# Performance work log

Hardware: AMD Instinct MI355X
Metric: run time of the kernel (lower is better)

## Reference

```python
import jax, jax.numpy as jnp
import numpy as np

B, S, D = 2, 2048, 1024
H, DK = 16, 64


def setup_inputs() -> dict:
    key = jax.random.key(0)
    ks = jax.random.split(key, 10)
    scale = D ** -0.5
    x = jax.random.normal(ks[0], (B, S, D), dtype=jnp.float32)
    mask = jax.random.randint(ks[1], (B, S), 0, 2) > 0  # True = masked positions
    Wq = jax.random.normal(ks[2], (D, H * DK), dtype=jnp.float32) * scale
    Wk = jax.random.normal(ks[3], (D, H * DK), dtype=jnp.float32) * scale
    Wv = jax.random.normal(ks[4], (D, H * DK), dtype=jnp.float32) * scale
    Wo = jax.random.normal(ks[5], (H * DK, D), dtype=jnp.float32) * scale
    bq = jnp.zeros((H * DK,), jnp.float32)
    bk = jnp.zeros((H * DK,), jnp.float32)
    bv = jnp.zeros((H * DK,), jnp.float32)
    bo = jnp.zeros((D,), jnp.float32)
    return {"x": x, "mask": mask, "Wq": Wq, "bq": bq, "Wk": Wk, "bk": bk,
            "Wv": Wv, "bv": bv, "Wo": Wo, "bo": bo}


def reference(x, mask, Wq, bq, Wk, bk, Wv, bv, Wo, bo):
    b, s, _ = x.shape
    # Linear + activation (dropout is identity at eval)
    q = jax.nn.relu(x @ Wq + bq).reshape(b, s, H, DK)
    k = jax.nn.relu(x @ Wk + bk).reshape(b, s, H, DK)
    v = jax.nn.relu(x @ Wv + bv).reshape(b, s, H, DK)
    # scores: [B, H, Sq, Sk]
    attn = jnp.einsum("bqhd,bkhd->bhqk", q, k) * (DK ** -0.5)
    # NOTE: original uses masked_fill(mask, 1e-9) BEFORE softmax (not -inf)
    attn = jnp.where(mask[:, None, None, :], jnp.float32(1e-9), attn)
    attn = jax.nn.softmax(attn, axis=-1)
    out = jnp.einsum("bhqk,bkhd->bqhd", attn, v).reshape(b, s, H * DK)
    return jax.nn.relu(out @ Wo + bo)
```

## Files before the change

### kernel.cpp

```cpp
#include <hip/hip_runtime.h>
#include <stdint.h>

typedef __attribute__((ext_vector_type(8))) short short8;
typedef __attribute__((ext_vector_type(4))) short short4b;
typedef __attribute__((ext_vector_type(4))) float f32x4;
typedef __attribute__((ext_vector_type(4))) unsigned short ushort4_t;

#define MFMA16(a, b, c) __builtin_amdgcn_mfma_f32_16x16x32_bf16((a), (b), (c), 0, 0, 0)

#if defined(__HIP_DEVICE_COMPILE__)
  #if __has_builtin(__builtin_amdgcn_mfma_f32_16x16x16bf16_1k)
    #define MFMA16K16(a, b, c) __builtin_amdgcn_mfma_f32_16x16x16bf16_1k((a), (b), (c), 0, 0, 0)
  #else
    #define MFMA16K16(a, b, c) __builtin_amdgcn_mfma_f32_16x16x16_bf16((a), (b), (c), 0, 0, 0)
  #endif
  #if __has_builtin(__builtin_amdgcn_exp2f)
    #define EXP2(x) __builtin_amdgcn_exp2f(x)
  #else
    #define EXP2(x) exp2f(x)
  #endif
#else
  #define MFMA16K16(a, b, c) (c)
  #define EXP2(x) exp2f(x)
#endif

#define SCL_F (0.125f * 1.44269504f)

__device__ __forceinline__ float b2f(unsigned short u) {
    union { unsigned u; float f; } c; c.u = ((unsigned)u) << 16; return c.f;
}
__device__ __forceinline__ unsigned short f2b(float f) {
    union { float f; unsigned u; } c; c.f = f;
    unsigned r = c.u + 0x7FFF + ((c.u >> 16) & 1);
    return (unsigned short)(r >> 16);
}
__device__ __forceinline__ unsigned f_as_u(float f) {
    union { float f; unsigned u; } c; c.f = f; return c.u;
}

__device__ __forceinline__ void g2lds16(const unsigned short* g, unsigned lds_byte_off) {
    __builtin_amdgcn_global_load_lds(
        (const __attribute__((address_space(1))) void*)(uintptr_t)g,
        (__attribute__((address_space(3))) void*)(uintptr_t)lds_byte_off,
        16, 0, 0);
}

__global__ void detect_dtype(const unsigned short* __restrict__ x, int* __restrict__ flag) {
    __shared__ int cnt;
    if (threadIdx.x == 0) cnt = 0;
    __syncthreads();
    int insane = 0;
    #pragma unroll
    for (int j = 0; j < 4; ++j) {
        unsigned short u = x[threadIdx.x * 4 + j];
        int e = (u >> 7) & 0xFF;
        if ((e >= 1 && e <= 90) || e >= 165) insane++;
    }
    atomicAdd(&cnt, insane);
    __syncthreads();
    if (threadIdx.x == 0) *flag = (cnt > 128) ? 1 : 0;
}

__global__ __launch_bounds__(256) void convtrans_k(const void* __restrict__ s0, const void* __restrict__ s1,
                                                   const void* __restrict__ s2, const void* __restrict__ s3,
                                                   const void* __restrict__ b0, const void* __restrict__ b1,
                                                   const void* __restrict__ b2, const void* __restrict__ b3s,
                                                   const void* __restrict__ xsrc,
                                                   unsigned short* __restrict__ xdst,
                                                   unsigned short* __restrict__ dstBase,
                                                   unsigned short* __restrict__ dstB3,
                                                   unsigned short* __restrict__ dstBo,
                                                   const int* __restrict__ flag) {
    const int z = blockIdx.z;
    if (z >= 5) {
        if (!*flag) return;
        const int slice = z - 5;
        const size_t i0 = (size_t)slice * 524288 + (blockIdx.y * 16 + blockIdx.x) * 2048 + threadIdx.x * 8;
        const float* s = (const float*)xsrc;
        float4 f0 = *(const float4*)&s[i0];
        float4 f1 = *(const float4*)&s[i0 + 4];
        unsigned short* t = &xdst[i0];
        t[0] = f2b(f0.x); t[1] = f2b(f0.y); t[2] = f2b(f0.z); t[3] = f2b(f0.w);
        t[4] = f2b(f1.x); t[5] = f2b(f1.y); t[6] = f2b(f1.z); t[7] = f2b(f1.w);
        return;
    }
    if (z == 4) {
        if (blockIdx.y != 0 || blockIdx.x >= 4) return;
        const int w = blockIdx.x;
        const void* src = (w == 0) ? b0 : (w == 1) ? b1 : (w == 2) ? b2 : b3s;
        const float bscl = (w == 0) ? SCL_F : 1.0f;
        #pragma unroll
        for (int j = 0; j < 4; ++j) {
            const int i = threadIdx.x * 4 + j;
            float fv = (*flag) ? ((const float*)src)[i] : b2f(((const unsigned short*)src)[i]);
            unsigned short v = f2b(fv * bscl);
            if (w < 3) dstB3[w * 1024 + i] = v;
            else dstBo[i] = v;
        }
        return;
    }
    __shared__ __align__(16) unsigned short tile[64 * 72];
    const void* src = (z == 0) ? s0 : (z == 1) ? s1 : (z == 2) ? s2 : s3;
    unsigned short* dst = dstBase + (size_t)z * 1024 * 1024;
    const float wscl = (z == 0) ? SCL_F : 1.0f;
    const int tid = threadIdx.x;
    const int r0 = blockIdx.y * 64, c0 = blockIdx.x * 64;
    const int rb = tid >> 3, c = (tid & 7) * 8;
    if (*flag) {
        const float* s = (const float*)src;
        #pragma unroll
        for (int it = 0; it < 2; ++it) {
            int rr = it * 32 + rb;
            float4 f0 = *(const float4*)&s[(size_t)(r0 + rr) * 1024 + c0 + c];
            float4 f1 = *(const float4*)&s[(size_t)(r0 + rr) * 1024 + c0 + c + 4];
            unsigned short* t = &tile[rr * 72 + c];
            t[0] = f2b(f0.x * wscl); t[1] = f2b(f0.y * wscl); t[2] = f2b(f0.z * wscl); t[3] = f2b(f0.w * wscl);
            t[4] = f2b(f1.x * wscl); t[5] = f2b(f1.y * wscl); t[6] = f2b(f1.z * wscl); t[7] = f2b(f1.w * wscl);
        }
    } else if (z == 0) {
        const unsigned short* s = (const unsigned short*)src;
        #pragma unroll
        for (int it = 0; it < 2; ++it) {
            int rr = it * 32 + rb;
            union { short8 v; unsigned short u[8]; } in;
            in.v = *(const short8*)&s[(size_t)(r0 + rr) * 1024 + c0 + c];
            unsigned short* t = &tile[rr * 72 + c];
            #pragma unroll
            for (int j = 0; j < 8; ++j) t[j] = f2b(b2f(in.u[j]) * SCL_F);
        }
    } else {
        const unsigned short* s = (const unsigned short*)src;
        #pragma unroll
        for (int it = 0; it < 2; ++it) {
            int rr = it * 32 + rb;
            *(short8*)&tile[rr * 72 + c] = *(const short8*)&s[(size_t)(r0 + rr) * 1024 + c0 + c];
        }
    }
    __syncthreads();
    #pragma unroll
    for (int it = 0; it < 2; ++it) {
        int n = it * 32 + rb, k8 = c;
        union { short8 s; unsigned short u[8]; } tmp;
        #pragma unroll
        for (int j = 0; j < 8; ++j) tmp.u[j] = tile[(k8 + j) * 72 + n];
        *(short8*)&dst[(size_t)(c0 + n) * 1024 + r0 + k8] = tmp.s;
    }
}

__global__ __launch_bounds__(256) void mask_k(unsigned short* __restrict__ qkv,
                                              const int* __restrict__ mask) {
    const int row = blockIdx.x * 2 + (threadIdx.x >> 7);
    const int col = (threadIdx.x & 127) * 8;
    if (mask[row]) {
        const short8 z = {0, 0, 0, 0, 0, 0, 0, 0};
        *(short8*)&qkv[(size_t)row * 3072 + 1024 + col] = z;
    }
}

__global__ __launch_bounds__(256) void gemm_bias_relu(const unsigned short* __restrict__ A,
                                                      const void* __restrict__ Araw,
                                                      const unsigned short* __restrict__ BT,
                                                      const unsigned short* __restrict__ bias,
                                                      void* __restrict__ C,
                                                      unsigned short* __restrict__ VtG,
                                                      const int* __restrict__ flag,
                                                      int M, int N, int K, int mode) {
    __shared__ __align__(16) unsigned short As[3][128 * 32];
    __shared__ __align__(16) unsigned short Bs[3][128 * 32];
    const int tid = threadIdx.x;
    const int wave = tid >> 6, lane = tid & 63;
    const int quad = lane >> 4, l16 = lane & 15;
    const int wm = wave >> 1, wn = wave & 1;
    const int m0 = blockIdx.y * 128, n0 = blockIdx.x * 128;

    const unsigned short* Ause = (Araw != nullptr && *flag == 0) ? (const unsigned short*)Araw : A;

    f32x4 acc[4][4];
    #pragma unroll
    for (int i = 0; i < 4; i++)
        #pragma unroll
        for (int j = 0; j < 4; j++) acc[i][j] = (f32x4){0.f, 0.f, 0.f, 0.f};

    const int srow = wave * 32 + (lane >> 2);
    const int sc8  = (lane & 3) * 8;
    const unsigned short* gA0 = Ause + (size_t)(m0 + srow) * K + sc8;
    const unsigned short* gA1 = gA0 + (size_t)16 * K;
    const unsigned short* gB0 = BT + (size_t)(n0 + srow) * K + sc8;
    const unsigned short* gB1 = gB0 + (size_t)16 * K;

    unsigned lA0 = (unsigned)(uintptr_t)&As[0][0] + wave * 2048;
    unsigned lA1 = (unsigned)(uintptr_t)&As[1][0] + wave * 2048;
    unsigned lA2 = (unsigned)(uintptr_t)&As[2][0] + wave * 2048;
    unsigned lB0 = (unsigned)(uintptr_t)&Bs[0][0] + wave * 2048;
    unsigned lB1 = (unsigned)(uintptr_t)&Bs[1][0] + wave * 2048;
    unsigned lB2 = (unsigned)(uintptr_t)&Bs[2][0] + wave * 2048;
    const unsigned short* pA0 = &As[0][0];
    const unsigned short* pA1 = &As[1][0];
    const unsigned short* pA2 = &As[2][0];
    const unsigned short* pB0 = &Bs[0][0];
    const unsigned short* pB1 = &Bs[1][0];
    const unsigned short* pB2 = &Bs[2][0];

    g2lds16(gA0, lA0); g2lds16(gA1, lA0 + 1024);
    g2lds16(gB0, lB0); g2lds16(gB1, lB0 + 1024);
    if (32 < K) {
        g2lds16(gA0 + 32, lA1); g2lds16(gA1 + 32, lA1 + 1024);
        g2lds16(gB0 + 32, lB1); g2lds16(gB1 + 32, lB1 + 1024);
    }
    if (64 < K) {
        g2lds16(gA0 + 64, lA2); g2lds16(gA1 + 64, lA2 + 1024);
        g2lds16(gB0 + 64, lB2); g2lds16(gB1 + 64, lB2 + 1024);
    }

    for (int k0 = 0; k0 < K; k0 += 32) {
        if (k0 + 64 < K)       asm volatile("s_waitcnt vmcnt(8)" ::: "memory");
        else if (k0 + 32 < K)  asm volatile("s_waitcnt vmcnt(4)" ::: "memory");
        else                   asm volatile("s_waitcnt vmcnt(0)" ::: "memory");
        __builtin_amdgcn_s_barrier();

        short8 af[4], bf[4];
        #pragma unroll
        for (int i = 0; i < 4; i++) af[i] = *(const short8*)&pA0[(wm * 64 + i * 16 + l16) * 32 + quad * 8];
        #pragma unroll
        for (int j = 0; j < 4; j++) bf[j] = *(const short8*)&pB0[(wn * 64 + j * 16 + l16) * 32 + quad * 8];
        #pragma unroll
        for (int i = 0; i < 4; i++)
            #pragma unroll
            for (int j = 0; j < 4; j++)
                acc[i][j] = MFMA16(af[i], bf[j], acc[i][j]);

        __builtin_amdgcn_s_barrier();

        if (k0 + 96 < K) {
            g2lds16(gA0 + k0 + 96, lA0); g2lds16(gA1 + k0 + 96, lA0 + 1024);
            g2lds16(gB0 + k0 + 96, lB0); g2lds16(gB1 + k0 + 96, lB0 + 1024);
        }
        unsigned tu;
        tu = lA0; lA0 = lA1; lA1 = lA2; lA2 = tu;
        tu = lB0; lB0 = lB1; lB1 = lB2; lB2 = tu;
        const unsigned short* tp;
        tp = pA0; pA0 = pA1; pA1 = pA2; pA2 = tp;
        tp = pB0; pB0 = pB1; pB1 = pB2; pB2 = tp;
    }

    if (mode == 2 && n0 >= 2048) {
        #pragma unroll
        for (int j = 0; j < 4; j++) {
            const int col = n0 + wn * 64 + j * 16 + l16;
            const int h  = (col - 2048) >> 6;
            const int dk = (col - 2048) & 63;
            const float bj = b2f(bias[col]);
            #pragma unroll
            for (int i = 0; i < 4; i++) {
                const int rowb = m0 + wm * 64 + i * 16 + quad * 4;
                const int bb = rowb >> 11;
                const int s0 = rowb & 2047;
                ushort4_t w;
                #pragma unroll
                for (int r = 0; r < 4; r++) {
                    float v = acc[i][j][r] + bj;
                    v = v > 0.f ? v : 0.f;
                    w[r] = f2b(v);
                }
                *(ushort4_t*)&VtG[(size_t)((bb * 16 + h) * 64 + dk) * 2048 + s0] = w;
            }
        }
    } else {
        const int f32out = (mode == 1) && (*flag != 0);
        #pragma unroll
        for (int j = 0; j < 4; j++) {
            const int col = n0 + wn * 64 + j * 16 + l16;
            const float bj = b2f(bias[col]);
            #pragma unroll
            for (int i = 0; i < 4; i++) {
                const int rowb = m0 + wm * 64 + i * 16 + quad * 4;
                #pragma unroll
                for (int r = 0; r < 4; r++) {
                    float v = acc[i][j][r] + bj;
                    v = v > 0.f ? v : 0.f;
                    if (f32out) ((float*)C)[(size_t)(rowb + r) * N + col] = v;
                    else ((unsigned short*)C)[(size_t)(rowb + r) * N + col] = f2b(v);
                }
            }
        }
    }
}

#define ATTN_TILE(Kbuf, Vbuf)                                                            \
    do {                                                                                 \
        __builtin_amdgcn_s_setprio(1);                                                   \
        f32x4 sA[4], sB[4];                                                              \
        _Pragma("unroll")                                                                \
        for (int t = 0; t < 4; ++t) {                                                    \
            const short8 kb0 = *(const short8*)&(Kbuf)[(((t * 16 + l16) * 64) + quad * 8) ^ rx];       \
            const short8 kb1 = *(const short8*)&(Kbuf)[(((t * 16 + l16) * 64) + 32 + quad * 8) ^ rx];  \
            f32x4 z = (f32x4){0.f, 0.f, 0.f, 0.f};                                       \
            sA[t] = MFMA16(kb1, qa1, MFMA16(kb0, qa0, z));                               \
            sB[t] = MFMA16(kb1, qb1, MFMA16(kb0, qb0, z));                               \
        }                                                                                \
        short4b vb[4][4];                                                                \
        _Pragma("unroll")                                                                \
        for (int t = 0; t < 4; ++t)                                                      \
            _Pragma("unroll")                                                            \
            for (int n = 0; n < 4; ++n)                                                  \
                vb[t][n] = *(const short4b*)&(Vbuf)[(((n * 16 + l16) * 64) + t * 16 + quad * 4) ^ rx]; \
        _Pragma("unroll")                                                                \
        for (int t = 0; t < 4; ++t) {                                                    \
            float pA[4], pB[4];                                                          \
            _Pragma("unroll")                                                            \
            for (int r = 0; r < 4; ++r) {                                                \
                pA[r] = EXP2(sA[t][r]);                                                  \
                pB[r] = EXP2(sB[t][r]);                                                  \
            }                                                                            \
            union { unsigned u[2]; short4b s; } fa, fb;                                  \
            fa.u[0] = __builtin_amdgcn_perm(f_as_u(pA[1]), f_as_u(pA[0]), 0x07060302u);  \
            fa.u[1] = __builtin_amdgcn_perm(f_as_u(pA[3]), f_as_u(pA[2]), 0x07060302u);  \
            fb.u[0] = __builtin_amdgcn_perm(f_as_u(pB[1]), f_as_u(pB[0]), 0x07060302u);  \
            fb.u[1] = __builtin_amdgcn_perm(f_as_u(pB[3]), f_as_u(pB[2]), 0x07060302u);  \
            _Pragma("unroll")                                                            \
            for (int n = 0; n < 4; ++n) {                                                \
                oA[n] = MFMA16K16(fa.s, vb[t][n], oA[n]);                                \
                oB[n] = MFMA16K16(fb.s, vb[t][n], oB[n]);                                \
            }                                                                            \
            sumA = MFMA16K16(fa.s, ones, sumA);                                          \
            sumB = MFMA16K16(fb.s, ones, sumB);                                          \
        }                                                                                \
        __builtin_amdgcn_s_setprio(0);                                                   \
    } while (0)

__global__ __launch_bounds__(256) void attn_kernel(const unsigned short* __restrict__ qkv,
                                                   const unsigned short* __restrict__ VtG,
                                                   unsigned short* __restrict__ out) {
    __shared__ __align__(16) unsigned short Ks[2][64 * 64];
    __shared__ __align__(16) unsigned short Vs[2][64 * 64];

    const int l = blockIdx.y * 16 + blockIdx.x;
    const int v = (l & 7) * 64 + (l >> 3);
    const int qt = v & 15, bh = v >> 4;
    const int b = bh >> 4, h = bh & 15;
    const int tid = threadIdx.x, wave = tid >> 6, lane = tid & 63;
    const int quad = lane >> 4, l16 = lane & 15;

    const int qrowA = qt * 128 + wave * 16 + l16;
    const unsigned short* qpA = qkv + (size_t)(b * 2048 + qrowA) * 3072 + h * 64;
    const unsigned short* qpB = qpA + (size_t)64 * 3072;
    const short8 qa0 = *(const short8*)(qpA + quad * 8);
    const short8 qa1 = *(const short8*)(qpA + 32 + quad * 8);
    const short8 qb0 = *(const short8*)(qpB + quad * 8);
    const short8 qb1 = *(const short8*)(qpB + 32 + quad * 8);

    f32x4 oA[4], oB[4], sumA, sumB;
    #pragma unroll
    for (int n = 0; n < 4; n++) { oA[n] = (f32x4){0.f,0.f,0.f,0.f}; oB[n] = (f32x4){0.f,0.f,0.f,0.f}; }
    sumA = (f32x4){0.f,0.f,0.f,0.f};
    sumB = (f32x4){0.f,0.f,0.f,0.f};

    const short4b ones = { (short)0x3F80, (short)0x3F80, (short)0x3F80, (short)0x3F80 };

    const int srow = tid >> 2;
    const int scol = (tid & 3) * 16;
    const int sxor = (srow & 7) << 3;
    const unsigned short* kg = qkv + (size_t)(b * 2048 + srow) * 3072 + 1024 + h * 64 + scol;
    const unsigned short* vg = VtG + (size_t)(bh * 64 + srow) * 2048 + scol;
    const size_t kstep = (size_t)64 * 3072;
    const int sidx0 = (srow * 64 + scol) ^ sxor;
    const int sidx1 = (srow * 64 + scol + 8) ^ sxor;
    unsigned short* wK0a = &Ks[0][sidx0];  unsigned short* wK1a = &Ks[0][sidx1];
    unsigned short* wV0a = &Vs[0][sidx0];  unsigned short* wV1a = &Vs[0][sidx1];
    unsigned short* wK0b = &Ks[1][sidx0];  unsigned short* wK1b = &Ks[1][sidx1];
    unsigned short* wV0b = &Vs[1][sidx0];  unsigned short* wV1b = &Vs[1][sidx1];

    const int rx = (l16 & 7) << 3;

    short8 rkA0 = *(const short8*)(kg);
    short8 rkA1 = *(const short8*)(kg + 8);
    short8 rvA0 = *(const short8*)(vg);
    short8 rvA1 = *(const short8*)(vg + 8);
    *(short8*)wK0a = rkA0;  *(short8*)wK1a = rkA1;
    *(short8*)wV0a = rvA0;  *(short8*)wV1a = rvA1;
    short8 rkB0 = *(const short8*)(kg + kstep);
    short8 rkB1 = *(const short8*)(kg + kstep + 8);
    short8 rvB0 = *(const short8*)(vg + 64);
    short8 rvB1 = *(const short8*)(vg + 64 + 8);
    __syncthreads();

    for (int kt = 0; kt < 32; kt += 2) {
        *(short8*)wK0b = rkB0;  *(short8*)wK1b = rkB1;
        *(short8*)wV0b = rvB0;  *(short8*)wV1b = rvB1;
        if (kt + 2 < 32) {
            rkA0 = *(const short8*)(kg + (kt + 2) * kstep);
            rkA1 = *(const short8*)(kg + (kt + 2) * kstep + 8);
            rvA0 = *(const short8*)(vg + (kt + 2) * 64);
            rvA1 = *(const short8*)(vg + (kt + 2) * 64 + 8);
        }
        ATTN_TILE(Ks[0], Vs[0]);
        __syncthreads();

        if (kt + 2 < 32) {
            *(short8*)wK0a = rkA0;  *(short8*)wK1a = rkA1;
            *(short8*)wV0a = rvA0;  *(short8*)wV1a = rvA1;
        }
        if (kt + 3 < 32) {
            rkB0 = *(const short8*)(kg + (kt + 3) * kstep);
            rkB1 = *(const short8*)(kg + (kt + 3) * kstep + 8);
            rvB0 = *(const short8*)(vg + (kt + 3) * 64);
            rvB1 = *(const short8*)(vg + (kt + 3) * 64 + 8);
        }
        ATTN_TILE(Ks[1], Vs[1]);
        __syncthreads();
    }

    float invA[4], invB[4];
    #pragma unroll
    for (int r = 0; r < 4; ++r) { invA[r] = 1.0f / sumA[r]; invB[r] = 1.0f / sumB[r]; }
    #pragma unroll
    for (int n = 0; n < 4; n++)
        #pragma unroll
        for (int r = 0; r < 4; r++) {
            const int row = qt * 128 + wave * 16 + quad * 4 + r;
            out[(size_t)(b * 2048 + row) * 1024 + h * 64 + n * 16 + l16] = f2b(oA[n][r] * invA[r]);
            out[(size_t)(b * 2048 + row + 64) * 1024 + h * 64 + n * 16 + l16] = f2b(oB[n][r] * invB[r]);
        }
}

extern "C" void kernel_launch(void* const* d_in, const int* in_sizes, int n_in,
                              void* d_out, int out_size, void* d_ws, size_t ws_size,
                              hipStream_t stream) {
    const void* x  = d_in[0];
    const int*  mk = (const int*)d_in[1];
    const void* Wq = d_in[2]; const void* bq = d_in[3];
    const void* Wk = d_in[4]; const void* bk = d_in[5];
    const void* Wv = d_in[6]; const void* bv = d_in[7];
    const void* Wo = d_in[8]; const void* bo = d_in[9];

    char* wsb = (char*)d_ws;
    int* flag = (int*)wsb;
    unsigned short* W0 = (unsigned short*)(wsb + 64);

    const size_t M1 = 1024u * 1024u;
    const size_t M4 = 4096u * 1024u;
    unsigned short* xb  = W0;
    unsigned short* WT  = xb + M4;
    unsigned short* WoT = WT + 3 * M1;
    unsigned short* b3  = WoT + M1;
    unsigned short* bob = b3 + 4096;
    unsigned short* qkv = bob + 1024;
    unsigned short* VtG = qkv + (size_t)4096 * 3072;
    unsigned short* abf = xb;

    detect_dtype<<<1, 256, 0, stream>>>((const unsigned short*)x, flag);

    convtrans_k<<<dim3(16, 16, 13), 256, 0, stream>>>(Wq, Wk, Wv, Wo, bq, bk, bv, bo,
                                                      x, xb, WT, b3, bob, flag);

    gemm_bias_relu<<<dim3(24, 32), 256, 0, stream>>>(xb, x, WT, b3, qkv, VtG, flag,
                                                     4096, 3072, 1024, 2);
    mask_k<<<2048, 256, 0, stream>>>(qkv, mk);
    attn_kernel<<<dim3(16, 32), 256, 0, stream>>>(qkv, VtG, abf);
    gemm_bias_relu<<<dim3(8, 32), 256, 0, stream>>>(abf, nullptr, WoT, bob, d_out, VtG, flag,
                                                    4096, 1024, 1024, 1);
}
```

Before: 197.2 us.

## Split attention key range across two wave groups and merge partial sums

The attention kernel now launches 512 threads per block, with two groups of four waves each handling half of the key sequence (16 tiles each) in separate double-buffered LDS regions. At the end, the second group writes its partial outputs and row sums to LDS, and the first group adds them and normalizes before storing. This is a split-K inside the block that doubles waves per block to improve latency hiding and occupancy on 512 blocks. The trade-off is doubled LDS use and an extra reduction step through shared memory. Merging partials without max rescaling is valid because the softmax is computed without a running max, using plain exp sums.

Result: slower. 205.1 us (+4.0%).

```diff
diff --git a/kernel.cpp b/kernel.cpp
--- a/kernel.cpp
+++ b/kernel.cpp
@@ -328,11 +328,11 @@
         __builtin_amdgcn_s_setprio(0);                                                   \
     } while (0)
 
-__global__ __launch_bounds__(256) void attn_kernel(const unsigned short* __restrict__ qkv,
+__global__ __launch_bounds__(512) void attn_kernel(const unsigned short* __restrict__ qkv,
                                                    const unsigned short* __restrict__ VtG,
                                                    unsigned short* __restrict__ out) {
-    __shared__ __align__(16) unsigned short Ks[2][64 * 64];
-    __shared__ __align__(16) unsigned short Vs[2][64 * 64];
+    __shared__ __align__(16) unsigned short Ks[2][2][64 * 64];
+    __shared__ __align__(16) unsigned short Vs[2][2][64 * 64];
 
     const int l = blockIdx.y * 16 + blockIdx.x;
     const int v = (l & 7) * 64 + (l >> 3);
@@ -340,8 +340,10 @@
     const int b = bh >> 4, h = bh & 15;
     const int tid = threadIdx.x, wave = tid >> 6, lane = tid & 63;
     const int quad = lane >> 4, l16 = lane & 15;
-
-    const int qrowA = qt * 128 + wave * 16 + l16;
+    const int hw = wave >> 2;
+    const int wq = wave & 3;
+
+    const int qrowA = qt * 128 + wq * 16 + l16;
     const unsigned short* qpA = qkv + (size_t)(b * 2048 + qrowA) * 3072 + h * 64;
     const unsigned short* qpB = qpA + (size_t)64 * 3072;
     const short8 qa0 = *(const short8*)(qpA + quad * 8);
@@ -357,70 +359,102 @@
 
     const short4b ones = { (short)0x3F80, (short)0x3F80, (short)0x3F80, (short)0x3F80 };
 
-    const int srow = tid >> 2;
-    const int scol = (tid & 3) * 16;
+    const int t256 = tid & 255;
+    const int srow = t256 >> 2;
+    const int scol = (t256 & 3) * 16;
     const int sxor = (srow & 7) << 3;
     const unsigned short* kg = qkv + (size_t)(b * 2048 + srow) * 3072 + 1024 + h * 64 + scol;
     const unsigned short* vg = VtG + (size_t)(bh * 64 + srow) * 2048 + scol;
     const size_t kstep = (size_t)64 * 3072;
+    const int tb = hw * 16;
     const int sidx0 = (srow * 64 + scol) ^ sxor;
     const int sidx1 = (srow * 64 + scol + 8) ^ sxor;
-    unsigned short* wK0a = &Ks[0][sidx0];  unsigned short* wK1a = &Ks[0][sidx1];
-    unsigned short* wV0a = &Vs[0][sidx0];  unsigned short* wV1a = &Vs[0][sidx1];
-    unsigned short* wK0b = &Ks[1][sidx0];  unsigned short* wK1b = &Ks[1][sidx1];
-    unsigned short* wV0b = &Vs[1][sidx0];  unsigned short* wV1b = &Vs[1][sidx1];
+    unsigned short* wK0a = &Ks[hw][0][sidx0];  unsigned short* wK1a = &Ks[hw][0][sidx1];
+    unsigned short* wV0a = &Vs[hw][0][sidx0];  unsigned short* wV1a = &Vs[hw][0][sidx1];
+    unsigned short* wK0b = &Ks[hw][1][sidx0];  unsigned short* wK1b = &Ks[hw][1][sidx1];
+    unsigned short* wV0b = &Vs[hw][1][sidx0];  unsigned short* wV1b = &Vs[hw][1][sidx1];
+    const unsigned short* rKa = &Ks[hw][0][0];
+    const unsigned short* rVa = &Vs[hw][0][0];
+    const unsigned short* rKb = &Ks[hw][1][0];
+    const unsigned short* rVb = &Vs[hw][1][0];
 
     const int rx = (l16 & 7) << 3;
 
-    short8 rkA0 = *(const short8*)(kg);
-    short8 rkA1 = *(const short8*)(kg + 8);
-    short8 rvA0 = *(const short8*)(vg);
-    short8 rvA1 = *(const short8*)(vg + 8);
+    short8 rkA0 = *(const short8*)(kg + (size_t)tb * kstep);
+    short8 rkA1 = *(const short8*)(kg + (size_t)tb * kstep + 8);
+    short8 rvA0 = *(const short8*)(vg + tb * 64);
+    short8 rvA1 = *(const short8*)(vg + tb * 64 + 8);
     *(short8*)wK0a = rkA0;  *(short8*)wK1a = rkA1;
     *(short8*)wV0a = rvA0;  *(short8*)wV1a = rvA1;
-    short8 rkB0 = *(const short8*)(kg + kstep);
-    short8 rkB1 = *(const short8*)(kg + kstep + 8);
-    short8 rvB0 = *(const short8*)(vg + 64);
-    short8 rvB1 = *(const short8*)(vg + 64 + 8);
+    short8 rkB0 = *(const short8*)(kg + (size_t)(tb + 1) * kstep);
+    short8 rkB1 = *(const short8*)(kg + (size_t)(tb + 1) * kstep + 8);
+    short8 rvB0 = *(const short8*)(vg + (tb + 1) * 64);
+    short8 rvB1 = *(const short8*)(vg + (tb + 1) * 64 + 8);
     __syncthreads();
 
-    for (int kt = 0; kt < 32; kt += 2) {
+    for (int kt = 0; kt < 16; kt += 2) {
         *(short8*)wK0b = rkB0;  *(short8*)wK1b = rkB1;
         *(short8*)wV0b = rvB0;  *(short8*)wV1b = rvB1;
-        if (kt + 2 < 32) {
-            rkA0 = *(const short8*)(kg + (kt + 2) * kstep);
-            rkA1 = *(const short8*)(kg + (kt + 2) * kstep + 8);
-            rvA0 = *(const short8*)(vg + (kt + 2) * 64);
-            rvA1 = *(const short8*)(vg + (kt + 2) * 64 + 8);
-        }
-        ATTN_TILE(Ks[0], Vs[0]);
+        if (kt + 2 < 16) {
+            rkA0 = *(const short8*)(kg + (size_t)(tb + kt + 2) * kstep);
+            rkA1 = *(const short8*)(kg + (size_t)(tb + kt + 2) * kstep + 8);
+            rvA0 = *(const short8*)(vg + (tb + kt + 2) * 64);
+            rvA1 = *(const short8*)(vg + (tb + kt + 2) * 64 + 8);
+        }
+        ATTN_TILE(rKa, rVa);
         __syncthreads();
 
-        if (kt + 2 < 32) {
+        if (kt + 2 < 16) {
             *(short8*)wK0a = rkA0;  *(short8*)wK1a = rkA1;
             *(short8*)wV0a = rvA0;  *(short8*)wV1a = rvA1;
         }
-        if (kt + 3 < 32) {
-            rkB0 = *(const short8*)(kg + (kt + 3) * kstep);
-            rkB1 = *(const short8*)(kg + (kt + 3) * kstep + 8);
-            rvB0 = *(const short8*)(vg + (kt + 3) * 64);
-            rvB1 = *(const short8*)(vg + (kt + 3) * 64 + 8);
-        }
-        ATTN_TILE(Ks[1], Vs[1]);
+        if (kt + 3 < 16) {
+            rkB0 = *(const short8*)(kg + (size_t)(tb + kt + 3) * kstep);
+            rkB1 = *(const short8*)(kg + (size_t)(tb + kt + 3) * kstep + 8);
+            rvB0 = *(const short8*)(vg + (tb + kt + 3) * 64);
+            rvB1 = *(const short8*)(vg + (tb + kt + 3) * 64 + 8);
+        }
+        ATTN_TILE(rKb, rVb);
         __syncthreads();
     }
 
-    float invA[4], invB[4];
-    #pragma unroll
-    for (int r = 0; r < 4; ++r) { invA[r] = 1.0f / sumA[r]; invB[r] = 1.0f / sumB[r]; }
-    #pragma unroll
-    for (int n = 0; n < 4; n++)
-        #pragma unroll
-        for (int r = 0; r < 4; r++) {
-            const int row = qt * 128 + wave * 16 + quad * 4 + r;
-            out[(size_t)(b * 2048 + row) * 1024 + h * 64 + n * 16 + l16] = f2b(oA[n][r] * invA[r]);
-            out[(size_t)(b * 2048 + row + 64) * 1024 + h * 64 + n * 16 + l16] = f2b(oB[n][r] * invB[r]);
-        }
+    float* OL = (float*)&Ks[0][0][0];
+    float* SL = (float*)&Vs[0][0][0];
+    if (hw == 1) {
+        #pragma unroll
+        for (int n = 0; n < 4; n++)
+            #pragma unroll
+            for (int r = 0; r < 4; r++) {
+                OL[(wq * 16 + quad * 4 + r) * 64 + n * 16 + l16] = oA[n][r];
+                OL[(64 + wq * 16 + quad * 4 + r) * 64 + n * 16 + l16] = oB[n][r];
+            }
+        if (l16 == 0) {
+            #pragma unroll
+            for (int r = 0; r < 4; r++) {
+                SL[wq * 16 + quad * 4 + r] = sumA[r];
+                SL[64 + wq * 16 + quad * 4 + r] = sumB[r];
+            }
+        }
+    }
+    __syncthreads();
+    if (hw == 0) {
+        float invA[4], invB[4];
+        #pragma unroll
+        for (int r = 0; r < 4; ++r) {
+            invA[r] = 1.0f / (sumA[r] + SL[wq * 16 + quad * 4 + r]);
+            invB[r] = 1.0f / (sumB[r] + SL[64 + wq * 16 + quad * 4 + r]);
+        }
+        #pragma unroll
+        for (int n = 0; n < 4; n++)
+            #pragma unroll
+            for (int r = 0; r < 4; r++) {
+                const float vA = oA[n][r] + OL[(wq * 16 + quad * 4 + r) * 64 + n * 16 + l16];
+                const float vB = oB[n][r] + OL[(64 + wq * 16 + quad * 4 + r) * 64 + n * 16 + l16];
+                const int row = qt * 128 + wq * 16 + quad * 4 + r;
+                out[(size_t)(b * 2048 + row) * 1024 + h * 64 + n * 16 + l16] = f2b(vA * invA[r]);
+                out[(size_t)(b * 2048 + row + 64) * 1024 + h * 64 + n * 16 + l16] = f2b(vB * invB[r]);
+            }
+    }
 }
 
 extern "C" void kernel_launch(void* const* d_in, const int* in_sizes, int n_in,
@@ -456,7 +490,7 @@
     gemm_bias_relu<<<dim3(24, 32), 256, 0, stream>>>(xb, x, WT, b3, qkv, VtG, flag,
                                                      4096, 3072, 1024, 2);
     mask_k<<<2048, 256, 0, stream>>>(qkv, mk);
-    attn_kernel<<<dim3(16, 32), 256, 0, stream>>>(qkv, VtG, abf);
+    attn_kernel<<<dim3(16, 32), 512, 0, stream>>>(qkv, VtG, abf);
     gemm_bias_relu<<<dim3(8, 32), 256, 0, stream>>>(abf, nullptr, WoT, bob, d_out, VtG, flag,
                                                     4096, 1024, 1024, 1);
 }
```
